# Kernel optimization log

Measured on AMD Instinct MI355X. Metric: run time of the kernel, lower is better.

Reference implementation:

```python
import jax, jax.numpy as jnp
import numpy as np

B, ISIZE, N, OSIZE = 2048, 512, 2048, 128
TC = 1.0 / 10.0  # dt/tau
PX = 0.5


def setup_inputs() -> dict:
    key = jax.random.key(0)
    ks = jax.random.split(key, 16)
    s = 0.01
    return {
        "x": jax.random.normal(ks[0], (B, ISIZE), jnp.float32),
        "h0_in": jax.random.normal(ks[1], (B, N), jnp.float32),
        "h1_in": jax.random.normal(ks[2], (B, N), jnp.float32),
        "h2_in": jax.random.normal(ks[3], (B, N), jnp.float32),
        "i_to_h0": s * jax.random.normal(ks[4], (ISIZE, N), jnp.float32),
        "h0_w": s * jax.random.normal(ks[5], (N, N), jnp.float32),
        "h0_b": s * jax.random.uniform(ks[6], (N,), jnp.float32),
        "h0_to_h1": s * jax.random.normal(ks[7], (N, N), jnp.float32),
        "h1_w": s * jax.random.normal(ks[8], (N, N), jnp.float32),
        "h1_b": s * jax.random.uniform(ks[9], (N,), jnp.float32),
        "h1_to_h2": s * jax.random.normal(ks[10], (N, N), jnp.float32),
        "h2_w": s * jax.random.normal(ks[11], (N, N), jnp.float32),
        "h2_b": s * jax.random.uniform(ks[12], (N,), jnp.float32),
        "w_out": s * jax.random.normal(ks[13], (N, OSIZE), jnp.float32),
        # Bernoulli(px) sparsity masks (non-trainable buffers in the original)
        "m01": (jax.random.uniform(ks[14], (N, N)) < PX).astype(jnp.float32),
        "m12": (jax.random.uniform(ks[15], (N, N)) < PX).astype(jnp.float32),
    }


def reference(x, h0_in, h1_in, h2_in, i_to_h0, h0_w, h0_b, h0_to_h1,
              h1_w, h1_b, h1_to_h2, h2_w, h2_b, w_out, m01, m12):
    tc = TC
    # zero-diagonal mask applied to every recurrent weight (no self-connections)
    diag = 1.0 - jnp.eye(N, dtype=h0_w.dtype)
    # replicate_ashok=True: feedforward weights are sparsified by Bernoulli masks
    h01 = h0_to_h1 * m01
    h12 = h1_to_h2 * m12

    # layer 0: input drive + masked recurrence + leaky integration
    h0 = h0_in * (1.0 - tc) + jax.nn.relu(
        x @ i_to_h0 + h0_in @ (h0_w * diag) + h0_b) * tc
    # layer 1
    h1 = h1_in * (1.0 - tc) + jax.nn.relu(
        h0 @ h01 + h1_in @ (h1_w * diag) + h1_b) * tc
    # layer 2
    h2 = h2_in * (1.0 - tc) + jax.nn.relu(
        h1 @ h12 + h2_in @ (h2_w * diag) + h2_b) * tc

    out = h2 @ w_out  # Linear without bias (replicate_ashok=True)
    return (h0, h1, h2, out)
```

## Files before the change

kernel.cpp:

```cpp
#include <hip/hip_runtime.h>
#include <hip/hip_bf16.h>
#include <stdint.h>

typedef __bf16 bf16;
typedef __bf16 bf16x8 __attribute__((ext_vector_type(8)));
typedef float f32x4 __attribute__((ext_vector_type(4)));

#define BB   2048
#define ISZ  512
#define NN   2048
#define OSZ  128

struct PackD { const float* src; bf16* dst; int W, ld, off, n8; };
struct TD    { const float* src; const float* msk; bf16* dst;
               int Ncols, ld_dst, k_off, mode, ntk, start; };
struct PAll  { PackD p[4]; TD d[7]; int packBlocks; };

__global__ __launch_bounds__(256) void prep_all_k(PAll a) {
  if ((int)blockIdx.x < a.packBlocks) {
    int idx = blockIdx.x * 256 + threadIdx.x;
    PackD d = a.p[0]; int base = 0;
#pragma unroll
    for (int i = 1; i < 4; ++i) if (idx >= a.p[i - 1].n8) { d = a.p[i]; base = a.p[i - 1].n8; }
    if (idx >= d.n8) return;
    int e = (idx - base) * 8;
    int m = e / d.W;
    int c = e - m * d.W;
    const float4 v0 = *reinterpret_cast<const float4*>(d.src + e);
    const float4 v1 = *reinterpret_cast<const float4*>(d.src + e + 4);
    bf16x8 o;
    o[0] = (bf16)v0.x; o[1] = (bf16)v0.y; o[2] = (bf16)v0.z; o[3] = (bf16)v0.w;
    o[4] = (bf16)v1.x; o[5] = (bf16)v1.y; o[6] = (bf16)v1.z; o[7] = (bf16)v1.w;
    *reinterpret_cast<bf16x8*>(d.dst + (size_t)m * d.ld + d.off + c) = o;
    return;
  }
  int bid = blockIdx.x - a.packBlocks;
  TD d = a.d[0];
#pragma unroll
  for (int i = 1; i < 7; ++i) if (bid >= a.d[i].start) d = a.d[i];
  int local = bid - d.start;
  int k0 = (local % d.ntk) * 128;
  int n0 = (local / d.ntk) * 32;
  __shared__ float t[128][33];
  const int tx8 = threadIdx.x & 7;
  const int kr  = threadIdx.x >> 3;
  const int nc  = n0 + tx8 * 4;
#pragma unroll
  for (int i = 0; i < 4; ++i) {
    int k = k0 + kr + 32 * i;
    float4 v = *reinterpret_cast<const float4*>(d.src + (size_t)k * d.Ncols + nc);
    if (d.mode == 2) {
      float4 m = *reinterpret_cast<const float4*>(d.msk + (size_t)k * d.Ncols + nc);
      v.x *= m.x; v.y *= m.y; v.z *= m.z; v.w *= m.w;
    } else if (d.mode == 1) {
      if (k == nc)     v.x = 0.f;
      if (k == nc + 1) v.y = 0.f;
      if (k == nc + 2) v.z = 0.f;
      if (k == nc + 3) v.w = 0.f;
    }
    float* r = &t[kr + 32 * i][tx8 * 4];
    r[0] = v.x; r[1] = v.y; r[2] = v.z; r[3] = v.w;
  }
  __syncthreads();
  const int n  = threadIdx.x >> 3;
  const int kc = (threadIdx.x & 7) * 16;
  bf16x8 o0, o1;
#pragma unroll
  for (int j = 0; j < 8; ++j) {
    o0[j] = (bf16)t[kc + j][n];
    o1[j] = (bf16)t[kc + 8 + j][n];
  }
  bf16* dp = d.dst + (size_t)(n0 + n) * d.ld_dst + d.k_off + k0 + kc;
  *reinterpret_cast<bf16x8*>(dp) = o0;
  *reinterpret_cast<bf16x8*>(dp + 8) = o1;
}

struct GP {
  const bf16* A; const bf16* B;
  int K, lda, ldb;
  const float* hin; const float* bias; const float* radd;
  float* outf; int ld_out;
  bf16* nxt; int ld_nxt;
  int epi;
};

__device__ __forceinline__ void gload16(const bf16* g, bf16* l) {
  __builtin_amdgcn_global_load_lds(
      (const __attribute__((address_space(1))) void*)g,
      (__attribute__((address_space(3))) void*)l, 16, 0, 0);
}

__device__ __forceinline__ void epilogue_store(const GP& p, int row, int col, float v) {
  size_t oidx = (size_t)row * p.ld_out + col;
  if (p.epi == 0) {
    float pre = v + p.bias[col];
    if (p.radd) pre += p.radd[oidx];
    float h = p.hin[oidx] * 0.9f + fmaxf(pre, 0.f) * 0.1f;
    p.outf[oidx] = h;
    p.nxt[(size_t)row * p.ld_nxt + col] = (bf16)h;
  } else {
    p.outf[oidx] = v;
  }
}

__device__ __forceinline__ void gemm_ks(const GP p) {
  __shared__ __align__(16) bf16 sm[2][2][128][64];
  const int lane = threadIdx.x & 63;
  const int wave = threadIdx.x >> 6;
  const int ks = wave >> 2;
  const int sp = wave & 3;
  const int gx = gridDim.x, nwg = gx * gridDim.y;
  const int lid = blockIdx.x + gx * blockIdx.y;
  const int q = nwg >> 3;
  const int swz = (lid & 7) * q + (lid >> 3);
  const int m0 = (swz / gx) * 128, n0 = (swz % gx) * 128;
  const int wm0 = (sp >> 1) * 64, wn0 = (sp & 1) * 64;
  const int srow = lane >> 3;
  const int scol = ((lane & 7) ^ srow) * 8;
  const int frow = lane & 15;
  const int rcol = (((ks << 2) + (lane >> 4)) ^ (frow & 7)) * 8;

  f32x4 acc[4][4];
#pragma unroll
  for (int i = 0; i < 4; ++i)
#pragma unroll
    for (int j = 0; j < 4; ++j)
#pragma unroll
      for (int r = 0; r < 4; ++r) acc[i][j][r] = 0.f;

  auto stage = [&](int buf, int t) {
    const int k0 = t * 64;
#pragma unroll
    for (int h = 0; h < 2; ++h) {
      const int c = wave + h * 8;
      gload16(p.A + (size_t)(m0 + c * 8 + srow) * p.lda + k0 + scol,
              &sm[buf][0][0][0] + c * 512);
      gload16(p.B + (size_t)(n0 + c * 8 + srow) * p.ldb + k0 + scol,
              &sm[buf][1][0][0] + c * 512);
    }
  };

  const int nt = p.K / 64;
  stage(0, 0);
  int cur = 0;
  for (int t = 0; t < nt; ++t) {
    if (t + 1 < nt) {
      stage(cur ^ 1, t + 1);
      asm volatile("s_waitcnt vmcnt(4)" ::: "memory");
    } else {
      asm volatile("s_waitcnt vmcnt(0)" ::: "memory");
    }
    __builtin_amdgcn_s_barrier();

    bf16x8 af[4], bf_[4];
#pragma unroll
    for (int i = 0; i < 4; ++i)
      af[i] = *reinterpret_cast<const bf16x8*>(&sm[cur][0][wm0 + i * 16 + frow][rcol]);
#pragma unroll
    for (int j = 0; j < 4; ++j)
      bf_[j] = *reinterpret_cast<const bf16x8*>(&sm[cur][1][wn0 + j * 16 + frow][rcol]);
#pragma unroll
    for (int i = 0; i < 4; ++i)
#pragma unroll
      for (int j = 0; j < 4; ++j)
        acc[i][j] = __builtin_amdgcn_mfma_f32_16x16x32_bf16(af[i], bf_[j], acc[i][j], 0, 0, 0);

    if (t + 1 < nt) {
      asm volatile("s_waitcnt lgkmcnt(0)" ::: "memory");
      __builtin_amdgcn_s_barrier();
    }
    cur ^= 1;
  }

  asm volatile("s_waitcnt lgkmcnt(0)" ::: "memory");
  __builtin_amdgcn_s_barrier();
  float* red = (float*)&sm[0][0][0][0];
  if (ks == 1) {
#pragma unroll
    for (int i = 0; i < 4; ++i)
#pragma unroll
      for (int j = 0; j < 4; ++j)
        *reinterpret_cast<f32x4*>(&red[sp * 4096 + (i * 4 + j) * 256 + lane * 4]) = acc[i][j];
    asm volatile("s_waitcnt lgkmcnt(0)" ::: "memory");
  }
  __builtin_amdgcn_s_barrier();
  if (ks == 0) {
#pragma unroll
    for (int i = 0; i < 4; ++i)
#pragma unroll
      for (int j = 0; j < 4; ++j) {
        f32x4 o = *reinterpret_cast<const f32x4*>(&red[sp * 4096 + (i * 4 + j) * 256 + lane * 4]);
#pragma unroll
        for (int r = 0; r < 4; ++r) acc[i][j][r] += o[r];
#pragma unroll
        for (int r = 0; r < 4; ++r)
          epilogue_store(p, m0 + wm0 + i * 16 + (lane >> 4) * 4 + r,
                         n0 + wn0 + j * 16 + (lane & 15), acc[i][j][r]);
      }
  }
}

template<int BM, int BN>
__device__ __forceinline__ void gemm_body8(const GP p) {
  constexpr int BK = 32;
  constexpr int WM = BM / 2, WN = BN / 4;
  constexpr int FM = WM / 16, FN = WN / 16;
  __shared__ bf16 As[2][BM][BK];
  __shared__ bf16 Bs[2][BN][BK];
  const int lane = threadIdx.x & 63;
  const int wave = threadIdx.x >> 6;
  const int m0 = blockIdx.y * BM, n0 = blockIdx.x * BN;
  const int wm0 = (wave >> 2) * WM, wn0 = (wave & 3) * WN;
  const int srow = lane >> 2;
  const int scolE = (((lane & 3) ^ ((lane >> 3) & 3)) * 8);
  const int frow = lane & 15;
  const int rcolE = (((lane >> 4) ^ ((frow >> 1) & 3)) * 8);

  f32x4 acc[FM][FN];
#pragma unroll
  for (int i = 0; i < FM; ++i)
#pragma unroll
    for (int j = 0; j < FN; ++j)
#pragma unroll
      for (int r = 0; r < 4; ++r) acc[i][j][r] = 0.f;

  auto stage = [&](int buf, int t) {
    const int k0 = t * BK;
#pragma unroll
    for (int c = wave; c < BM / 16; c += 8) {
      const bf16* g = p.A + (size_t)(m0 + c * 16 + srow) * p.lda + k0 + scolE;
      gload16(g, &As[buf][0][0] + c * 512);
    }
#pragma unroll
    for (int c = wave; c < BN / 16; c += 8) {
      const bf16* g = p.B + (size_t)(n0 + c * 16 + srow) * p.ldb + k0 + scolE;
      gload16(g, &Bs[buf][0][0] + c * 512);
    }
  };

  const int nt = p.K / BK;
  stage(0, 0);
  __syncthreads();
  int cur = 0;
  for (int t = 0; t < nt; ++t) {
    if (t + 1 < nt) stage(cur ^ 1, t + 1);
    bf16x8 af[FM], bfrag[FN];
#pragma unroll
    for (int i = 0; i < FM; ++i)
      af[i] = *reinterpret_cast<const bf16x8*>(&As[cur][wm0 + i * 16 + frow][rcolE]);
#pragma unroll
    for (int j = 0; j < FN; ++j)
      bfrag[j] = *reinterpret_cast<const bf16x8*>(&Bs[cur][wn0 + j * 16 + frow][rcolE]);
#pragma unroll
    for (int i = 0; i < FM; ++i)
#pragma unroll
      for (int j = 0; j < FN; ++j)
        acc[i][j] = __builtin_amdgcn_mfma_f32_16x16x32_bf16(af[i], bfrag[j], acc[i][j], 0, 0, 0);
    __syncthreads();
    cur ^= 1;
  }

#pragma unroll
  for (int i = 0; i < FM; ++i)
#pragma unroll
    for (int j = 0; j < FN; ++j)
#pragma unroll
      for (int r = 0; r < 4; ++r)
        epilogue_store(p, m0 + wm0 + i * 16 + (lane >> 4) * 4 + r,
                       n0 + wn0 + j * 16 + (lane & 15), acc[i][j][r]);
}

__global__ __launch_bounds__(512) void k_tri(GP p0, GP p1, GP p2) {
  GP p;
  if (blockIdx.z == 0) p = p0;
  else if (blockIdx.z == 1) p = p1;
  else p = p2;
  gemm_ks(p);
}

__global__ __launch_bounds__(512) void k_split(GP p0, GP p1) {
  gemm_ks(blockIdx.z == 0 ? p0 : p1);
}

__global__ __launch_bounds__(512) void k_out(GP p) { gemm_body8<32, 64>(p); }

__global__ __launch_bounds__(256) void k_epi(const float* __restrict__ P0,
                                             const float* __restrict__ P1,
                                             const float* __restrict__ radd,
                                             const float* __restrict__ hin,
                                             const float* __restrict__ bias,
                                             float* __restrict__ outf,
                                             bf16* __restrict__ nxt) {
  int e = (blockIdx.x * 256 + threadIdx.x) * 8;
  int colb = e & (NN - 1);
  const float4 a0 = *reinterpret_cast<const float4*>(P0 + e);
  const float4 a1 = *reinterpret_cast<const float4*>(P0 + e + 4);
  const float4 b0 = *reinterpret_cast<const float4*>(P1 + e);
  const float4 b1 = *reinterpret_cast<const float4*>(P1 + e + 4);
  const float4 r0 = *reinterpret_cast<const float4*>(radd + e);
  const float4 r1 = *reinterpret_cast<const float4*>(radd + e + 4);
  const float4 h0 = *reinterpret_cast<const float4*>(hin + e);
  const float4 h1 = *reinterpret_cast<const float4*>(hin + e + 4);
  const float4 c0 = *reinterpret_cast<const float4*>(bias + colb);
  const float4 c1 = *reinterpret_cast<const float4*>(bias + colb + 4);
  float pa[8] = {a0.x, a0.y, a0.z, a0.w, a1.x, a1.y, a1.z, a1.w};
  float pb[8] = {b0.x, b0.y, b0.z, b0.w, b1.x, b1.y, b1.z, b1.w};
  float pr[8] = {r0.x, r0.y, r0.z, r0.w, r1.x, r1.y, r1.z, r1.w};
  float ph[8] = {h0.x, h0.y, h0.z, h0.w, h1.x, h1.y, h1.z, h1.w};
  float pc[8] = {c0.x, c0.y, c0.z, c0.w, c1.x, c1.y, c1.z, c1.w};
  float4 o0, o1;
  bf16x8 nb;
#pragma unroll
  for (int j = 0; j < 8; ++j) {
    float pre = pa[j] + pb[j] + pr[j] + pc[j];
    float h = ph[j] * 0.9f + fmaxf(pre, 0.f) * 0.1f;
    (j < 4 ? (&o0.x)[j] : (&o1.x)[j - 4]) = h;
    nb[j] = (bf16)h;
  }
  *reinterpret_cast<float4*>(outf + e) = o0;
  *reinterpret_cast<float4*>(outf + e + 4) = o1;
  *reinterpret_cast<bf16x8*>(nxt + e) = nb;
}

extern "C" void kernel_launch(void* const* d_in, const int* in_sizes, int n_in,
                              void* d_out, int out_size, void* d_ws, size_t ws_size,
                              hipStream_t stream) {
  const float* x        = (const float*)d_in[0];
  const float* h0_in    = (const float*)d_in[1];
  const float* h1_in    = (const float*)d_in[2];
  const float* h2_in    = (const float*)d_in[3];
  const float* i_to_h0  = (const float*)d_in[4];
  const float* h0_w     = (const float*)d_in[5];
  const float* h0_b     = (const float*)d_in[6];
  const float* h0_to_h1 = (const float*)d_in[7];
  const float* h1_w     = (const float*)d_in[8];
  const float* h1_b     = (const float*)d_in[9];
  const float* h1_to_h2 = (const float*)d_in[10];
  const float* h2_w     = (const float*)d_in[11];
  const float* h2_b     = (const float*)d_in[12];
  const float* w_out    = (const float*)d_in[13];
  const float* m01      = (const float*)d_in[14];
  const float* m12      = (const float*)d_in[15];
  float* out = (float*)d_out;

  uint8_t* ws = (uint8_t*)d_ws;
  constexpr size_t OFF_A0  = 0;
  constexpr size_t OFF_W0  = OFF_A0 + 10485760;
  constexpr size_t OFF_W1R = OFF_W0 + 10485760;
  constexpr size_t OFF_W2R = OFF_W1R + 8388608;
  constexpr size_t OFF_W01 = OFF_W2R + 8388608;
  constexpr size_t OFF_W12 = OFF_W01 + 8388608;
  constexpr size_t OFF_WO  = OFF_W12 + 8388608;
  constexpr size_t OFF_AR1 = OFF_WO + 524288;
  constexpr size_t OFF_AR2 = OFF_AR1 + 8388608;
  constexpr size_t OFF_AH0 = OFF_AR2 + 8388608;
  constexpr size_t WS_NEED = OFF_AH0 + 8388608;
  if (ws_size < WS_NEED) return;

  bf16* A0  = (bf16*)(ws + OFF_A0);
  bf16* Wt0 = (bf16*)(ws + OFF_W0);
  bf16* W1r = (bf16*)(ws + OFF_W1R);
  bf16* W2r = (bf16*)(ws + OFF_W2R);
  bf16* W01 = (bf16*)(ws + OFF_W01);
  bf16* W12 = (bf16*)(ws + OFF_W12);
  bf16* WtO = (bf16*)(ws + OFF_WO);
  bf16* Ar1 = (bf16*)(ws + OFF_AR1);
  bf16* Ar2 = (bf16*)(ws + OFF_AR2);
  bf16* Ah0 = (bf16*)(ws + OFF_AH0);
  bf16* Ah1 = Ar1;
  bf16* Ah2 = Ar2;
  float* P0 = (float*)(ws + 0);
  float* P1 = (float*)(ws + 16777216);

  float* o_h0  = out;
  float* o_h1  = out + (size_t)BB * NN;
  float* o_h2  = out + (size_t)2 * BB * NN;
  float* o_out = out + (size_t)3 * BB * NN;

  PAll pa;
  int n8a = BB * ISZ / 8;
  int n8b = n8a + BB * NN / 8;
  int n8c = n8b + BB * NN / 8;
  int n8d = n8c + BB * NN / 8;
  pa.p[0] = {x,     A0,  ISZ, ISZ + NN, 0,   n8a};
  pa.p[1] = {h0_in, A0,  NN,  ISZ + NN, ISZ, n8b};
  pa.p[2] = {h1_in, Ar1, NN,  NN,       0,   n8c};
  pa.p[3] = {h2_in, Ar2, NN,  NN,       0,   n8d};
  pa.packBlocks = (n8d + 255) / 256;
  int s0 = 0;
  pa.d[0] = {i_to_h0,  nullptr, Wt0, NN,  ISZ + NN, 0,   0, ISZ / 128, s0}; s0 += (ISZ / 128) * (NN / 32);
  pa.d[1] = {h0_w,     nullptr, Wt0, NN,  ISZ + NN, ISZ, 1, NN / 128,  s0}; s0 += (NN / 128) * (NN / 32);
  pa.d[2] = {h1_w,     nullptr, W1r, NN,  NN,       0,   1, NN / 128,  s0}; s0 += (NN / 128) * (NN / 32);
  pa.d[3] = {h2_w,     nullptr, W2r, NN,  NN,       0,   1, NN / 128,  s0}; s0 += (NN / 128) * (NN / 32);
  pa.d[4] = {h0_to_h1, m01,     W01, NN,  NN,       0,   2, NN / 128,  s0}; s0 += (NN / 128) * (NN / 32);
  pa.d[5] = {h1_to_h2, m12,     W12, NN,  NN,       0,   2, NN / 128,  s0}; s0 += (NN / 128) * (NN / 32);
  pa.d[6] = {w_out,    nullptr, WtO, OSZ, NN,       0,   0, NN / 128,  s0}; s0 += (NN / 128) * (OSZ / 32);
  prep_all_k<<<pa.packBlocks + s0, 256, 0, stream>>>(pa);

  GP pS0{A0,  Wt0, ISZ + NN, ISZ + NN, ISZ + NN, h0_in, h0_b, nullptr,
         o_h0, NN, Ah0, NN, 0};
  GP pR1{Ar1, W1r, NN, NN, NN, nullptr, nullptr, nullptr, o_h1, NN, nullptr, 0, 1};
  GP pR2{Ar2, W2r, NN, NN, NN, nullptr, nullptr, nullptr, o_h2, NN, nullptr, 0, 1};
  k_tri<<<dim3(NN / 128, BB / 128, 3), 512, 0, stream>>>(pS0, pR1, pR2);

  GP pG1a{Ah0,          W01,          NN / 2, NN, NN, nullptr, nullptr, nullptr, P0, NN, nullptr, 0, 1};
  GP pG1b{Ah0 + NN / 2, W01 + NN / 2, NN / 2, NN, NN, nullptr, nullptr, nullptr, P1, NN, nullptr, 0, 1};
  k_split<<<dim3(NN / 128, BB / 128, 2), 512, 0, stream>>>(pG1a, pG1b);
  k_epi<<<BB * NN / 2048, 256, 0, stream>>>(P0, P1, o_h1, h1_in, h1_b, o_h1, Ah1);

  GP pG2a{Ah1,          W12,          NN / 2, NN, NN, nullptr, nullptr, nullptr, P0, NN, nullptr, 0, 1};
  GP pG2b{Ah1 + NN / 2, W12 + NN / 2, NN / 2, NN, NN, nullptr, nullptr, nullptr, P1, NN, nullptr, 0, 1};
  k_split<<<dim3(NN / 128, BB / 128, 2), 512, 0, stream>>>(pG2a, pG2b);
  k_epi<<<BB * NN / 2048, 256, 0, stream>>>(P0, P1, o_h2, h2_in, h2_b, o_h2, Ah2);

  GP pO{Ah2, WtO, NN, NN, NN, nullptr, nullptr, nullptr, o_out, OSZ, nullptr, 0, 1};
  k_out<<<dim3(OSZ / 64, BB / 32), 512, 0, stream>>>(pO);
}
```

Measured before the change: 215.5 us.

## Overlap masked feedforward and output weight transposes with first GEMM launch

Moves the mask-multiply, transpose and bf16 conversion of h0_to_h1, h1_to_h2 and w_out out of the prep kernel and into an extra z-slice of the k_tri launch. That slice runs alongside the layer-0 and recurrent GEMMs and shares a raw 64KB LDS buffer with them. The aim is to shrink the serial prep kernel and hide the weight-conversion traffic behind compute-bound GEMM work. In exchange, the tail of k_tri can get longer, and the extra blocks compete with the GEMM blocks for CUs and memory bandwidth. The transpose code also contains a redundant, oddly written first load of o0.

```diff
diff --git a/kernel.cpp b/kernel.cpp
--- a/kernel.cpp
+++ b/kernel.cpp
@@ -15,6 +15,7 @@
 struct TD    { const float* src; const float* msk; bf16* dst;
                int Ncols, ld_dst, k_off, mode, ntk, start; };
 struct PAll  { PackD p[4]; TD d[7]; int packBlocks; };
+struct TDef  { TD d[3]; int total; };
 
 __global__ __launch_bounds__(256) void prep_all_k(PAll a) {
   if ((int)blockIdx.x < a.packBlocks) {
@@ -103,8 +104,9 @@
   }
 }
 
-__device__ __forceinline__ void gemm_ks(const GP p) {
-  __shared__ __align__(16) bf16 sm[2][2][128][64];
+__device__ __forceinline__ void gemm_ks(const GP p, uint8_t* smraw) {
+  typedef bf16 smT[2][128][64];
+  smT* sm = (smT*)smraw;
   const int lane = threadIdx.x & 63;
   const int wave = threadIdx.x >> 6;
   const int ks = wave >> 2;
@@ -174,7 +176,7 @@
 
   asm volatile("s_waitcnt lgkmcnt(0)" ::: "memory");
   __builtin_amdgcn_s_barrier();
-  float* red = (float*)&sm[0][0][0][0];
+  float* red = (float*)smraw;
   if (ks == 1) {
 #pragma unroll
     for (int i = 0; i < 4; ++i)
@@ -198,6 +200,74 @@
                          n0 + wn0 + j * 16 + (lane & 15), acc[i][j][r]);
       }
   }
+}
+
+__device__ __forceinline__ void transpose512(const TD& d, int tile, bool active,
+                                             uint8_t* smraw) {
+  float (*t)[65] = (float (*)[65])smraw;
+  int k0 = 0, n0 = 0;
+  if (active) { k0 = (tile % d.ntk) * 128; n0 = (tile / d.ntk) * 64; }
+  const int tx = threadIdx.x & 15;
+  const int kr = threadIdx.x >> 4;
+  const int nc = n0 + tx * 4;
+  if (active) {
+#pragma unroll
+    for (int i = 0; i < 4; ++i) {
+      int k = k0 + kr + 32 * i;
+      float4 v = *reinterpret_cast<const float4*>(d.src + (size_t)k * d.Ncols + nc);
+      if (d.mode == 2) {
+        float4 m = *reinterpret_cast<const float4*>(d.msk + (size_t)k * d.Ncols + nc);
+        v.x *= m.x; v.y *= m.y; v.z *= m.z; v.w *= m.w;
+      }
+      float* r = &t[kr + 32 * i][tx * 4];
+      r[0] = v.x; r[1] = v.y; r[2] = v.z; r[3] = v.w;
+    }
+  }
+  __syncthreads();
+  if (active) {
+    const int n  = threadIdx.x >> 3;
+    const int kc = (threadIdx.x & 7) * 16;
+    bf16x8 o0, o1;
+#pragma unroll
+    for (int j = 0; j < 8; ++j) {
+      o0[j] = (bf16)t[kc + j][n0 + n - n0 + n * 0 + n];
+      o1[j] = (bf16)t[kc + 8 + j][n];
+    }
+#pragma unroll
+    for (int j = 0; j < 8; ++j) o0[j] = (bf16)t[kc + j][n];
+    bf16* dp = d.dst + (size_t)(n0 + n) * d.ld_dst + d.k_off + k0 + kc;
+    *reinterpret_cast<bf16x8*>(dp) = o0;
+    *reinterpret_cast<bf16x8*>(dp + 8) = o1;
+  }
+  __syncthreads();
+}
+
+__global__ __launch_bounds__(512) void k_tri(GP p0, GP p1, GP p2, TDef td) {
+  __shared__ __align__(16) uint8_t smraw[65536];
+  if (blockIdx.z < 3) {
+    GP p;
+    if (blockIdx.z == 0) p = p0;
+    else if (blockIdx.z == 1) p = p1;
+    else p = p2;
+    gemm_ks(p, smraw);
+    return;
+  }
+  const int bid = blockIdx.x + gridDim.x * blockIdx.y;
+  const int nb = gridDim.x * gridDim.y;
+  const int iters = (td.total + nb - 1) / nb;
+  for (int it = 0; it < iters; ++it) {
+    int tile = it * nb + bid;
+    TD d = td.d[0];
+    if (tile >= td.d[1].start) d = td.d[1];
+    if (tile >= td.d[2].start) d = td.d[2];
+    int local = tile - d.start;
+    transpose512(d, local, tile < td.total, smraw);
+  }
+}
+
+__global__ __launch_bounds__(512) void k_split(GP p0, GP p1) {
+  __shared__ __align__(16) uint8_t smraw[65536];
+  gemm_ks(blockIdx.z == 0 ? p0 : p1, smraw);
 }
 
 template<int BM, int BN>
@@ -268,18 +338,6 @@
       for (int r = 0; r < 4; ++r)
         epilogue_store(p, m0 + wm0 + i * 16 + (lane >> 4) * 4 + r,
                        n0 + wn0 + j * 16 + (lane & 15), acc[i][j][r]);
-}
-
-__global__ __launch_bounds__(512) void k_tri(GP p0, GP p1, GP p2) {
-  GP p;
-  if (blockIdx.z == 0) p = p0;
-  else if (blockIdx.z == 1) p = p1;
-  else p = p2;
-  gemm_ks(p);
-}
-
-__global__ __launch_bounds__(512) void k_split(GP p0, GP p1) {
-  gemm_ks(blockIdx.z == 0 ? p0 : p1);
 }
 
 __global__ __launch_bounds__(512) void k_out(GP p) { gemm_body8<32, 64>(p); }
@@ -388,20 +446,27 @@
   pa.p[3] = {h2_in, Ar2, NN,  NN,       0,   n8d};
   pa.packBlocks = (n8d + 255) / 256;
   int s0 = 0;
-  pa.d[0] = {i_to_h0,  nullptr, Wt0, NN,  ISZ + NN, 0,   0, ISZ / 128, s0}; s0 += (ISZ / 128) * (NN / 32);
-  pa.d[1] = {h0_w,     nullptr, Wt0, NN,  ISZ + NN, ISZ, 1, NN / 128,  s0}; s0 += (NN / 128) * (NN / 32);
-  pa.d[2] = {h1_w,     nullptr, W1r, NN,  NN,       0,   1, NN / 128,  s0}; s0 += (NN / 128) * (NN / 32);
-  pa.d[3] = {h2_w,     nullptr, W2r, NN,  NN,       0,   1, NN / 128,  s0}; s0 += (NN / 128) * (NN / 32);
-  pa.d[4] = {h0_to_h1, m01,     W01, NN,  NN,       0,   2, NN / 128,  s0}; s0 += (NN / 128) * (NN / 32);
-  pa.d[5] = {h1_to_h2, m12,     W12, NN,  NN,       0,   2, NN / 128,  s0}; s0 += (NN / 128) * (NN / 32);
-  pa.d[6] = {w_out,    nullptr, WtO, OSZ, NN,       0,   0, NN / 128,  s0}; s0 += (NN / 128) * (OSZ / 32);
+  pa.d[0] = {i_to_h0, nullptr, Wt0, NN, ISZ + NN, 0,   0, ISZ / 128, s0}; s0 += (ISZ / 128) * (NN / 32);
+  pa.d[1] = {h0_w,    nullptr, Wt0, NN, ISZ + NN, ISZ, 1, NN / 128,  s0}; s0 += (NN / 128) * (NN / 32);
+  pa.d[2] = {h1_w,    nullptr, W1r, NN, NN,       0,   1, NN / 128,  s0}; s0 += (NN / 128) * (NN / 32);
+  pa.d[3] = {h2_w,    nullptr, W2r, NN, NN,       0,   1, NN / 128,  s0}; s0 += (NN / 128) * (NN / 32);
+  pa.d[4] = pa.d[3]; pa.d[4].start = 0x7FFFFFFF;
+  pa.d[5] = pa.d[4];
+  pa.d[6] = pa.d[4];
   prep_all_k<<<pa.packBlocks + s0, 256, 0, stream>>>(pa);
+
+  TDef td;
+  int t0 = 0;
+  td.d[0] = {h0_to_h1, m01, W01, NN,  NN, 0, 2, NN / 128, t0}; t0 += (NN / 128) * (NN / 64);
+  td.d[1] = {h1_to_h2, m12, W12, NN,  NN, 0, 2, NN / 128, t0}; t0 += (NN / 128) * (NN / 64);
+  td.d[2] = {w_out,  nullptr, WtO, OSZ, NN, 0, 0, NN / 128, t0}; t0 += (NN / 128) * (OSZ / 64);
+  td.total = t0;
 
   GP pS0{A0,  Wt0, ISZ + NN, ISZ + NN, ISZ + NN, h0_in, h0_b, nullptr,
          o_h0, NN, Ah0, NN, 0};
   GP pR1{Ar1, W1r, NN, NN, NN, nullptr, nullptr, nullptr, o_h1, NN, nullptr, 0, 1};
   GP pR2{Ar2, W2r, NN, NN, NN, nullptr, nullptr, nullptr, o_h2, NN, nullptr, 0, 1};
-  k_tri<<<dim3(NN / 128, BB / 128, 3), 512, 0, stream>>>(pS0, pR1, pR2);
+  k_tri<<<dim3(NN / 128, BB / 128, 4), 512, 0, stream>>>(pS0, pR1, pR2, td);
 
   GP pG1a{Ah0,          W01,          NN / 2, NN, NN, nullptr, nullptr, nullptr, P0, NN, nullptr, 0, 1};
   GP pG1b{Ah0 + NN / 2, W01 + NN / 2, NN / 2, NN, NN, nullptr, nullptr, nullptr, P1, NN, nullptr, 0, 1};
```

Result: no change. 214.4 us (median of 2 runs) (-0.5%).
